# Kernel optimization log

Hardware: AMD Instinct MI355X
Metric: run time of the kernel (lower is better)

Reference implementation:

```python
import jax, jax.numpy as jnp
import numpy as np

B, N, E, F, H = 4, 10000, 320000, 128, 128


def setup_inputs() -> dict:
    key = jax.random.key(0)
    ks = jax.random.split(key, 12)
    s = 1.0 / np.sqrt(F)
    sh = 1.0 / np.sqrt(H)
    return {
        "batch_feat": jax.random.normal(ks[0], (B, N, F), dtype=jnp.float32),
        "batch_edges": jax.random.randint(ks[1], (B, 2, E), 0, N, dtype=jnp.int32),
        "batch_attr": jax.random.uniform(ks[2], (B, E), dtype=jnp.float32),
        "W1": jax.random.uniform(ks[3], (F, H), jnp.float32, -s, s),
        "b1": jnp.zeros((H,), jnp.float32),
        "W2": jax.random.uniform(ks[4], (H, H), jnp.float32, -sh, sh),
        "b2": jnp.zeros((H,), jnp.float32),
        "W3": jax.random.uniform(ks[5], (H, H), jnp.float32, -sh, sh),
        "b3": jnp.zeros((H,), jnp.float32),
        "Wl": jax.random.uniform(ks[6], (H, 1), jnp.float32, -sh, sh),
        "bl": jnp.zeros((1,), jnp.float32),
    }


def reference(batch_feat, batch_edges, batch_attr, W1, b1, W2, b2, W3, b3, Wl, bl):
    n_nodes = batch_feat.shape[1]

    def gcn_conv(x, row, col, w, W, b):
        # PyG gcn_norm with add_self_loops=False: deg = scatter_add(w, col)
        deg = jax.ops.segment_sum(w, col, num_segments=n_nodes)  # [N]
        dinv = jnp.where(deg > 0, jax.lax.rsqrt(deg), 0.0)
        norm = dinv[row] * w * dinv[col]                         # [E]
        xw = x @ W                                               # [N,H]
        msg = norm[:, None] * xw[row]                            # gather [E,H]
        return jax.ops.segment_sum(msg, col, num_segments=n_nodes) + b

    def per_graph(x, ei, w):
        row, col = ei[0], ei[1]
        h = jax.nn.relu(gcn_conv(x, row, col, w, W1, b1))
        h = jax.nn.relu(gcn_conv(h, row, col, w, W2, b2))
        h = jax.nn.relu(gcn_conv(h, row, col, w, W3, b3))
        return h.mean(axis=0) @ Wl + bl                          # [1]

    return jax.vmap(per_graph)(batch_feat, batch_edges, batch_attr)  # [B,1]
```

## Files before the change

kernel.cpp:

```cpp
#include <hip/hip_runtime.h>

#define BB 4
#define NN 10000
#define EE 320000
#define HH 128
#define HALFN 5000
#define NK2 (2 * NN)
#define RS (2 * NN + 1)

__global__ __launch_bounds__(256) void rank_kernel(
    const int* __restrict__ edges, int* __restrict__ cnt, int* __restrict__ rank) {
  int b = blockIdx.y;
  int e0 = (blockIdx.x * 256 + threadIdx.x) * 2;
  int2 rr = *(const int2*)(edges + (size_t)b * 2 * EE + e0);
  int2 cc = *(const int2*)(edges + (size_t)b * 2 * EE + EE + e0);
  int k0 = ((rr.x >= HALFN) ? NN : 0) + cc.x;
  int k1 = ((rr.y >= HALFN) ? NN : 0) + cc.y;
  int r0 = atomicAdd(&cnt[b * NK2 + k0], 1);
  int r1 = atomicAdd(&cnt[b * NK2 + k1], 1);
  *(int2*)(rank + (size_t)b * EE + e0) = make_int2(r0, r1);
}

__global__ __launch_bounds__(256) void scan_kernel(
    const int* __restrict__ cnt, int* __restrict__ rowstart) {
  int b = blockIdx.x, t = threadIdx.x;
  __shared__ int s[256];
  int running = 0;
  for (int base = 0; base < NK2; base += 2048) {
    int v[8];
    int i0 = base + t * 8;
    int tsum = 0;
#pragma unroll
    for (int j = 0; j < 8; ++j) {
      v[j] = (i0 + j < NK2) ? cnt[b * NK2 + i0 + j] : 0;
      tsum += v[j];
    }
    s[t] = tsum;
    __syncthreads();
    for (int o = 1; o < 256; o <<= 1) {
      int add = (t >= o) ? s[t - o] : 0;
      __syncthreads();
      s[t] += add;
      __syncthreads();
    }
    int ex = running + s[t] - tsum;
#pragma unroll
    for (int j = 0; j < 8; ++j) {
      if (i0 + j < NK2) rowstart[b * RS + i0 + j] = ex;
      ex += v[j];
    }
    int tot = s[255];
    __syncthreads();
    running += tot;
  }
  if (t == 0) rowstart[b * RS + NK2] = running;
}

__global__ __launch_bounds__(256) void fill_kernel(
    const int* __restrict__ edges, const float* __restrict__ attr,
    const int* __restrict__ rank, const int* __restrict__ rowstart,
    int2* __restrict__ csr) {
  int b = blockIdx.y;
  int e0 = (blockIdx.x * 256 + threadIdx.x) * 2;
  int2 rr = *(const int2*)(edges + (size_t)b * 2 * EE + e0);
  int2 cc = *(const int2*)(edges + (size_t)b * 2 * EE + EE + e0);
  float2 ww = *(const float2*)(attr + (size_t)b * EE + e0);
  int2 rk = *(const int2*)(rank + (size_t)b * EE + e0);
  int k0 = ((rr.x >= HALFN) ? NN : 0) + cc.x;
  int k1 = ((rr.y >= HALFN) ? NN : 0) + cc.y;
  int p0 = rowstart[b * RS + k0] + rk.x;
  int p1 = rowstart[b * RS + k1] + rk.y;
  csr[(size_t)b * EE + p0] = make_int2(rr.x, __float_as_int(ww.x));
  csr[(size_t)b * EE + p1] = make_int2(rr.y, __float_as_int(ww.y));
}

__global__ __launch_bounds__(256) void deg_kernel(
    const int2* __restrict__ csr, const int* __restrict__ rowstart,
    float* __restrict__ dinv) {
  int b = blockIdx.y;
  int n = blockIdx.x * 256 + threadIdx.x;
  if (n >= NN) return;
  const int2* c = csr + (size_t)b * EE;
  float sum = 0.f;
#pragma unroll
  for (int q = 0; q < 2; ++q) {
    int key = q * NN + n;
    int s0 = rowstart[b * RS + key], s1 = rowstart[b * RS + key + 1];
    for (int i = s0; i < s1; ++i) sum += __int_as_float(c[i].y);
  }
  dinv[b * NN + n] = sum > 0.f ? rsqrtf(sum) : 0.f;
}

__global__ __launch_bounds__(256) void norm_kernel(
    int2* __restrict__ csr, const int* __restrict__ rowstart,
    const float* __restrict__ dinv) {
  int b = blockIdx.y;
  int n = blockIdx.x * 4 + (threadIdx.x >> 6);
  int lane = threadIdx.x & 63;
  float dc = dinv[b * NN + n];
  int2* c = csr + (size_t)b * EE;
#pragma unroll
  for (int q = 0; q < 2; ++q) {
    int key = q * NN + n;
    int s0 = rowstart[b * RS + key], s1 = rowstart[b * RS + key + 1];
    for (int i = s0 + lane; i < s1; i += 64) {
      int2 e = c[i];
      c[i].y = __float_as_int(dc * __int_as_float(e.y) * dinv[b * NN + e.x]);
    }
  }
}

__global__ __launch_bounds__(256) void gemm_kernel(
    const float* __restrict__ x, const float* __restrict__ W,
    float* __restrict__ out) {
  __shared__ float xs[32 * 68];
  __shared__ float ws[32 * 144];
  int b = blockIdx.y;
  int row0 = blockIdx.x * 64;
  int t = threadIdx.x;
  int rg = t >> 4, cg = t & 15;
  int fc = cg * 8 + ((cg >> 2) << 2);
  float acc[4][8];
#pragma unroll
  for (int r = 0; r < 4; ++r)
#pragma unroll
    for (int j = 0; j < 8; ++j) acc[r][j] = 0.f;
  const float* xb = x + (size_t)b * NN * HH;

  for (int k0 = 0; k0 < HH; k0 += 32) {
#pragma unroll
    for (int i = 0; i < 2; ++i) {
      int idx = t + i * 256;
      int rl = idx >> 3, kq = idx & 7;
      int row = row0 + rl;
      float4 v = make_float4(0.f, 0.f, 0.f, 0.f);
      if (row < NN) v = *(const float4*)(xb + (size_t)row * HH + k0 + kq * 4);
      xs[(kq * 4 + 0) * 68 + rl] = v.x;
      xs[(kq * 4 + 1) * 68 + rl] = v.y;
      xs[(kq * 4 + 2) * 68 + rl] = v.z;
      xs[(kq * 4 + 3) * 68 + rl] = v.w;
    }
#pragma unroll
    for (int i = 0; i < 4; ++i) {
      int idx = t + i * 256;
      int kk = idx >> 5, c = (idx & 31) * 4;
      float4 v = *(const float4*)(W + (size_t)(k0 + kk) * HH + c);
      int f = c + ((c >> 5) << 2);
      *(float4*)&ws[kk * 144 + f] = v;
    }
    __syncthreads();
#pragma unroll 4
    for (int k = 0; k < 32; ++k) {
      float4 xv = *(const float4*)&xs[k * 68 + rg * 4];
      float4 w0 = *(const float4*)&ws[k * 144 + fc];
      float4 w1 = *(const float4*)&ws[k * 144 + fc + 4];
      const float* xp = (const float*)&xv;
#pragma unroll
      for (int r = 0; r < 4; ++r) {
        acc[r][0] += xp[r] * w0.x; acc[r][1] += xp[r] * w0.y;
        acc[r][2] += xp[r] * w0.z; acc[r][3] += xp[r] * w0.w;
        acc[r][4] += xp[r] * w1.x; acc[r][5] += xp[r] * w1.y;
        acc[r][6] += xp[r] * w1.z; acc[r][7] += xp[r] * w1.w;
      }
    }
    __syncthreads();
  }
#pragma unroll
  for (int r = 0; r < 4; ++r) {
    int row = row0 + rg * 4 + r;
    if (row < NN) {
      float* og = out + ((size_t)b * NN + row) * HH + cg * 8;
      *(float4*)og = make_float4(acc[r][0], acc[r][1], acc[r][2], acc[r][3]);
      *(float4*)(og + 4) = make_float4(acc[r][4], acc[r][5], acc[r][6], acc[r][7]);
    }
  }
}

__global__ __launch_bounds__(256) void agg_kernel(
    const float* __restrict__ xw, const int2* __restrict__ csr,
    const int* __restrict__ rowstart, const float* __restrict__ bias,
    float* __restrict__ h, int phase) {
  int g = blockIdx.x & 7;
  int b = g >> 1;
  int q = g & 1;
  int chunk = blockIdx.x >> 3;
  int nhalf = (phase == 0) ? q : 1 - q;
  int half = (threadIdx.x >> 5) & 1;
  int n = nhalf * HALFN + chunk * 8 + (threadIdx.x >> 6) * 2 + half;
  int sl = threadIdx.x & 31;
  int key = q * NN + n;
  int s0 = rowstart[b * RS + key], s1 = rowstart[b * RS + key + 1];
  const float* xwg = xw + (size_t)b * NN * HH;
  const int2* c = csr + (size_t)b * EE;
  float4 a0 = make_float4(0.f, 0.f, 0.f, 0.f);
  float4 a1 = make_float4(0.f, 0.f, 0.f, 0.f);
  int i = s0;
  for (; i + 2 <= s1; i += 2) {
    int2 e0 = c[i];
    int2 e1 = c[i + 1];
    float4 v0 = *(const float4*)(xwg + (size_t)e0.x * HH + sl * 4);
    float4 v1 = *(const float4*)(xwg + (size_t)e1.x * HH + sl * 4);
    float w0 = __int_as_float(e0.y);
    float w1 = __int_as_float(e1.y);
    a0.x += w0 * v0.x; a0.y += w0 * v0.y; a0.z += w0 * v0.z; a0.w += w0 * v0.w;
    a1.x += w1 * v1.x; a1.y += w1 * v1.y; a1.z += w1 * v1.z; a1.w += w1 * v1.w;
  }
  if (i < s1) {
    int2 e0 = c[i];
    float4 v0 = *(const float4*)(xwg + (size_t)e0.x * HH + sl * 4);
    float w0 = __int_as_float(e0.y);
    a0.x += w0 * v0.x; a0.y += w0 * v0.y; a0.z += w0 * v0.z; a0.w += w0 * v0.w;
  }
  a0.x += a1.x; a0.y += a1.y; a0.z += a1.z; a0.w += a1.w;
  float* hp = h + ((size_t)b * NN + n) * HH + sl * 4;
  if (phase == 0) {
    *(float4*)hp = a0;
  } else {
    float4 prev = *(const float4*)hp;
    float4 bb = *(const float4*)(bias + sl * 4);
    *(float4*)hp = make_float4(fmaxf(prev.x + a0.x + bb.x, 0.f),
                               fmaxf(prev.y + a0.y + bb.y, 0.f),
                               fmaxf(prev.z + a0.z + bb.z, 0.f),
                               fmaxf(prev.w + a0.w + bb.w, 0.f));
  }
}

__global__ __launch_bounds__(64) void init_out_kernel(float* out, const float* __restrict__ bl) {
  if (threadIdx.x < BB) out[threadIdx.x] = bl[0];
}

__global__ __launch_bounds__(256) void final_kernel(
    const float* __restrict__ h, const float* __restrict__ Wl,
    float* __restrict__ out) {
  int b = blockIdx.y;
  int t = threadIdx.x;
  int f = t & 127;
  int rr = t >> 7;
  float p = 0.f;
  for (int n = blockIdx.x * 2 + rr; n < NN; n += gridDim.x * 2)
    p += h[((size_t)b * NN + n) * HH + f];
  __shared__ float s[256];
  s[t] = p;
  __syncthreads();
  float v = 0.f;
  if (t < 128) v = (s[t] + s[t + 128]) * Wl[f];
  __syncthreads();
  s[t] = v;
  __syncthreads();
  for (int o = 64; o > 0; o >>= 1) {
    if (t < o) s[t] += s[t + o];
    __syncthreads();
  }
  if (t == 0) atomicAdd(&out[b], s[0] * (1.0f / NN));
}

extern "C" void kernel_launch(void* const* d_in, const int* in_sizes, int n_in,
                              void* d_out, int out_size, void* d_ws, size_t ws_size,
                              hipStream_t stream) {
  const float* feat = (const float*)d_in[0];
  const int* edges = (const int*)d_in[1];
  const float* attr = (const float*)d_in[2];
  const float* W1 = (const float*)d_in[3];
  const float* b1 = (const float*)d_in[4];
  const float* W2 = (const float*)d_in[5];
  const float* b2 = (const float*)d_in[6];
  const float* W3 = (const float*)d_in[7];
  const float* b3 = (const float*)d_in[8];
  const float* Wl = (const float*)d_in[9];
  const float* bl = (const float*)d_in[10];
  float* out = (float*)d_out;

  char* ws = (char*)d_ws;
  size_t off = 0;
  auto alloc = [&](size_t bytes) {
    size_t o = off;
    off = (off + bytes + 255) & ~(size_t)255;
    return o;
  };
  int*   cnt      = (int*)  (ws + alloc((size_t)BB * NK2 * 4));
  int*   rowstart = (int*)  (ws + alloc((size_t)BB * RS * 4));
  int2*  csr      = (int2*) (ws + alloc((size_t)BB * EE * 8));
  float* xw       = (float*)(ws + alloc((size_t)BB * NN * HH * 4));
  float* h        = (float*)(ws + alloc((size_t)BB * NN * HH * 4));
  int*   rank = (int*)xw;
  float* dinv = (float*)h;

  (void)hipMemsetAsync(cnt, 0, (size_t)BB * NK2 * 4, stream);

  dim3 egrid2(EE / 512, BB);
  rank_kernel<<<egrid2, 256, 0, stream>>>(edges, cnt, rank);
  scan_kernel<<<BB, 256, 0, stream>>>(cnt, rowstart);
  fill_kernel<<<egrid2, 256, 0, stream>>>(edges, attr, rank, rowstart, csr);
  deg_kernel<<<dim3((NN + 255) / 256, BB), 256, 0, stream>>>(csr, rowstart, dinv);
  norm_kernel<<<dim3(NN / 4, BB), 256, 0, stream>>>(csr, rowstart, dinv);

  dim3 ggrid((NN + 63) / 64, BB);
  int agrid = 8 * (HALFN / 8);

  gemm_kernel<<<ggrid, 256, 0, stream>>>(feat, W1, xw);
  agg_kernel<<<agrid, 256, 0, stream>>>(xw, csr, rowstart, b1, h, 0);
  agg_kernel<<<agrid, 256, 0, stream>>>(xw, csr, rowstart, b1, h, 1);
  gemm_kernel<<<ggrid, 256, 0, stream>>>(h, W2, xw);
  agg_kernel<<<agrid, 256, 0, stream>>>(xw, csr, rowstart, b2, h, 0);
  agg_kernel<<<agrid, 256, 0, stream>>>(xw, csr, rowstart, b2, h, 1);
  gemm_kernel<<<ggrid, 256, 0, stream>>>(h, W3, xw);
  agg_kernel<<<agrid, 256, 0, stream>>>(xw, csr, rowstart, b3, h, 0);
  agg_kernel<<<agrid, 256, 0, stream>>>(xw, csr, rowstart, b3, h, 1);

  init_out_kernel<<<1, 64, 0, stream>>>(out, bl);
  final_kernel<<<dim3(64, BB), 256, 0, stream>>>(h, Wl, out);
}
```

Measured before the change: 391.2 us.

## Fold GCN normalization into aggregation and unroll edge loop by four

Removes the separate norm_kernel pass that rewrote every CSR edge weight with dinv[row]*w*dinv[col]. The aggregation now multiplies each raw edge weight by dinv of the source node as it gathers, and applies the destination dinv once per node in the final phase. dinv moves into the count buffer so it stays live across the later kernels. The edge loop is also unrolled from two to four independent accumulators to keep more gathers in flight. In exchange, each edge does an extra small gather of dinv in every layer, and registers per thread go up.

Measured after the change: 381.9 us. 1.02x faster.

```diff
diff --git a/kernel.cpp b/kernel.cpp
--- a/kernel.cpp
+++ b/kernel.cpp
@@ -91,25 +91,6 @@
   dinv[b * NN + n] = sum > 0.f ? rsqrtf(sum) : 0.f;
 }
 
-__global__ __launch_bounds__(256) void norm_kernel(
-    int2* __restrict__ csr, const int* __restrict__ rowstart,
-    const float* __restrict__ dinv) {
-  int b = blockIdx.y;
-  int n = blockIdx.x * 4 + (threadIdx.x >> 6);
-  int lane = threadIdx.x & 63;
-  float dc = dinv[b * NN + n];
-  int2* c = csr + (size_t)b * EE;
-#pragma unroll
-  for (int q = 0; q < 2; ++q) {
-    int key = q * NN + n;
-    int s0 = rowstart[b * RS + key], s1 = rowstart[b * RS + key + 1];
-    for (int i = s0 + lane; i < s1; i += 64) {
-      int2 e = c[i];
-      c[i].y = __float_as_int(dc * __int_as_float(e.y) * dinv[b * NN + e.x]);
-    }
-  }
-}
-
 __global__ __launch_bounds__(256) void gemm_kernel(
     const float* __restrict__ x, const float* __restrict__ W,
     float* __restrict__ out) {
@@ -178,8 +159,8 @@
 
 __global__ __launch_bounds__(256) void agg_kernel(
     const float* __restrict__ xw, const int2* __restrict__ csr,
-    const int* __restrict__ rowstart, const float* __restrict__ bias,
-    float* __restrict__ h, int phase) {
+    const int* __restrict__ rowstart, const float* __restrict__ dinv,
+    const float* __restrict__ bias, float* __restrict__ h, int phase) {
   int g = blockIdx.x & 7;
   int b = g >> 1;
   int q = g & 1;
@@ -191,37 +172,52 @@
   int key = q * NN + n;
   int s0 = rowstart[b * RS + key], s1 = rowstart[b * RS + key + 1];
   const float* xwg = xw + (size_t)b * NN * HH;
+  const float* dv = dinv + b * NN;
   const int2* c = csr + (size_t)b * EE;
   float4 a0 = make_float4(0.f, 0.f, 0.f, 0.f);
   float4 a1 = make_float4(0.f, 0.f, 0.f, 0.f);
+  float4 a2 = make_float4(0.f, 0.f, 0.f, 0.f);
+  float4 a3 = make_float4(0.f, 0.f, 0.f, 0.f);
   int i = s0;
-  for (; i + 2 <= s1; i += 2) {
+  for (; i + 4 <= s1; i += 4) {
     int2 e0 = c[i];
     int2 e1 = c[i + 1];
+    int2 e2 = c[i + 2];
+    int2 e3 = c[i + 3];
+    float w0 = __int_as_float(e0.y) * dv[e0.x];
+    float w1 = __int_as_float(e1.y) * dv[e1.x];
+    float w2 = __int_as_float(e2.y) * dv[e2.x];
+    float w3 = __int_as_float(e3.y) * dv[e3.x];
     float4 v0 = *(const float4*)(xwg + (size_t)e0.x * HH + sl * 4);
     float4 v1 = *(const float4*)(xwg + (size_t)e1.x * HH + sl * 4);
-    float w0 = __int_as_float(e0.y);
-    float w1 = __int_as_float(e1.y);
+    float4 v2 = *(const float4*)(xwg + (size_t)e2.x * HH + sl * 4);
+    float4 v3 = *(const float4*)(xwg + (size_t)e3.x * HH + sl * 4);
     a0.x += w0 * v0.x; a0.y += w0 * v0.y; a0.z += w0 * v0.z; a0.w += w0 * v0.w;
     a1.x += w1 * v1.x; a1.y += w1 * v1.y; a1.z += w1 * v1.z; a1.w += w1 * v1.w;
-  }
-  if (i < s1) {
+    a2.x += w2 * v2.x; a2.y += w2 * v2.y; a2.z += w2 * v2.z; a2.w += w2 * v2.w;
+    a3.x += w3 * v3.x; a3.y += w3 * v3.y; a3.z += w3 * v3.z; a3.w += w3 * v3.w;
+  }
+  for (; i < s1; ++i) {
     int2 e0 = c[i];
+    float w0 = __int_as_float(e0.y) * dv[e0.x];
     float4 v0 = *(const float4*)(xwg + (size_t)e0.x * HH + sl * 4);
-    float w0 = __int_as_float(e0.y);
     a0.x += w0 * v0.x; a0.y += w0 * v0.y; a0.z += w0 * v0.z; a0.w += w0 * v0.w;
   }
-  a0.x += a1.x; a0.y += a1.y; a0.z += a1.z; a0.w += a1.w;
+  a0.x += a1.x + a2.x + a3.x;
+  a0.y += a1.y + a2.y + a3.y;
+  a0.z += a1.z + a2.z + a3.z;
+  a0.w += a1.w + a2.w + a3.w;
   float* hp = h + ((size_t)b * NN + n) * HH + sl * 4;
   if (phase == 0) {
     *(float4*)hp = a0;
   } else {
+    float dn = dv[n];
     float4 prev = *(const float4*)hp;
     float4 bb = *(const float4*)(bias + sl * 4);
-    *(float4*)hp = make_float4(fmaxf(prev.x + a0.x + bb.x, 0.f),
-                               fmaxf(prev.y + a0.y + bb.y, 0.f),
-                               fmaxf(prev.z + a0.z + bb.z, 0.f),
-                               fmaxf(prev.w + a0.w + bb.w, 0.f));
+    *(float4*)hp = make_float4(fmaxf((prev.x + a0.x) * dn + bb.x, 0.f),
+                               fmaxf((prev.y + a0.y) * dn + bb.y, 0.f),
+                               fmaxf((prev.z + a0.z) * dn + bb.z, 0.f),
+                               fmaxf((prev.w + a0.w) * dn + bb.w, 0.f));
   }
 }
 
@@ -283,7 +279,7 @@
   float* xw       = (float*)(ws + alloc((size_t)BB * NN * HH * 4));
   float* h        = (float*)(ws + alloc((size_t)BB * NN * HH * 4));
   int*   rank = (int*)xw;
-  float* dinv = (float*)h;
+  float* dinv = (float*)cnt;
 
   (void)hipMemsetAsync(cnt, 0, (size_t)BB * NK2 * 4, stream);
 
@@ -292,20 +288,19 @@
   scan_kernel<<<BB, 256, 0, stream>>>(cnt, rowstart);
   fill_kernel<<<egrid2, 256, 0, stream>>>(edges, attr, rank, rowstart, csr);
   deg_kernel<<<dim3((NN + 255) / 256, BB), 256, 0, stream>>>(csr, rowstart, dinv);
-  norm_kernel<<<dim3(NN / 4, BB), 256, 0, stream>>>(csr, rowstart, dinv);
 
   dim3 ggrid((NN + 63) / 64, BB);
   int agrid = 8 * (HALFN / 8);
 
   gemm_kernel<<<ggrid, 256, 0, stream>>>(feat, W1, xw);
-  agg_kernel<<<agrid, 256, 0, stream>>>(xw, csr, rowstart, b1, h, 0);
-  agg_kernel<<<agrid, 256, 0, stream>>>(xw, csr, rowstart, b1, h, 1);
+  agg_kernel<<<agrid, 256, 0, stream>>>(xw, csr, rowstart, dinv, b1, h, 0);
+  agg_kernel<<<agrid, 256, 0, stream>>>(xw, csr, rowstart, dinv, b1, h, 1);
   gemm_kernel<<<ggrid, 256, 0, stream>>>(h, W2, xw);
-  agg_kernel<<<agrid, 256, 0, stream>>>(xw, csr, rowstart, b2, h, 0);
-  agg_kernel<<<agrid, 256, 0, stream>>>(xw, csr, rowstart, b2, h, 1);
+  agg_kernel<<<agrid, 256, 0, stream>>>(xw, csr, rowstart, dinv, b2, h, 0);
+  agg_kernel<<<agrid, 256, 0, stream>>>(xw, csr, rowstart, dinv, b2, h, 1);
   gemm_kernel<<<ggrid, 256, 0, stream>>>(h, W3, xw);
-  agg_kernel<<<agrid, 256, 0, stream>>>(xw, csr, rowstart, b3, h, 0);
-  agg_kernel<<<agrid, 256, 0, stream>>>(xw, csr, rowstart, b3, h, 1);
+  agg_kernel<<<agrid, 256, 0, stream>>>(xw, csr, rowstart, dinv, b3, h, 0);
+  agg_kernel<<<agrid, 256, 0, stream>>>(xw, csr, rowstart, dinv, b3, h, 1);
 
   init_out_kernel<<<1, 64, 0, stream>>>(out, bl);
   final_kernel<<<dim3(64, BB), 256, 0, stream>>>(h, Wl, out);
```
